# Kernel optimization log

Measured on AMD Instinct MI355X. Metric: run time of the kernel, lower is better.

## Reference

```python
import jax, jax.numpy as jnp
import numpy as np

N_HEAD = 16
ROPE_BASE = 10000.0

def rotate_half(x):
    half = x.shape[-1] // 2
    return jnp.concatenate((-x[..., half:], x[..., :half]), axis=-1)

def rope_freqs(T, head_dim, dtype):
    inv_freq = 1.0 / (ROPE_BASE ** (jnp.arange(0, head_dim, 2, dtype=jnp.float32) / head_dim))
    t = jnp.arange(T, dtype=jnp.float32)
    freqs = t[:, None] * inv_freq[None, :]          # [T, head_dim//2]
    emb = jnp.concatenate((freqs, freqs), axis=-1)  # [T, head_dim]
    return emb.astype(dtype)

def setup_inputs() -> dict:
    key = jax.random.key(0)
    ks = jax.random.split(key, 9)
    B, T, C = 2, 2048, 1024
    s = 1.0 / np.sqrt(C)
    return {
        'x':  jax.random.normal(ks[0], (B, T, C), jnp.float32),
        'Wq': jax.random.normal(ks[1], (C, C), jnp.float32) * s,
        'bq': jnp.zeros((C,), jnp.float32),
        'Wk': jax.random.normal(ks[2], (C, C), jnp.float32) * s,
        'bk': jnp.zeros((C,), jnp.float32),
        'Wv': jax.random.normal(ks[3], (C, C), jnp.float32) * s,
        'bv': jnp.zeros((C,), jnp.float32),
        'Wp': jax.random.normal(ks[4], (C, C), jnp.float32) * s,
        'bp': jnp.zeros((C,), jnp.float32),
    }

def reference(x, Wq, bq, Wk, bk, Wv, bv, Wp, bp):
    B, T, C = x.shape
    H = N_HEAD
    D = C // H
    # torch Linear: y = x @ W.T + b
    def heads(y):
        return y.reshape(B, T, H, D).transpose(0, 2, 1, 3)  # [B,H,T,D]
    q = heads(x @ Wq.T + bq)
    k = heads(x @ Wk.T + bk)
    v = heads(x @ Wv.T + bv)
    # inline RoPE
    emb = rope_freqs(T, D, x.dtype)          # [T, D]
    cos, sin = jnp.cos(emb), jnp.sin(emb)
    q = q * cos + rotate_half(q) * sin
    k = k * cos + rotate_half(k) * sin
    # full T x T scores with causal masked softmax
    att = jnp.einsum('bhtd,bhsd->bhts', q, k) * (1.0 / jnp.sqrt(jnp.array(D, x.dtype)))
    causal = jnp.tril(jnp.ones((T, T), bool))
    att = jnp.where(causal[None, None], att, jnp.array(-jnp.inf, att.dtype))
    att = jax.nn.softmax(att, axis=-1)
    y = jnp.einsum('bhts,bhsd->bhtd', att, v)  # [B,H,T,D]
    y = y.transpose(0, 2, 1, 3).reshape(B, T, C)
    return y @ Wp.T + bp
```

## Files before the change

### kernel.cpp

```cpp
#include <hip/hip_runtime.h>
#include <hip/hip_bf16.h>
#include <stdint.h>

typedef unsigned short u16;
typedef __attribute__((ext_vector_type(8))) short bf16x8;
typedef __attribute__((ext_vector_type(4))) float f32x4;
typedef __attribute__((ext_vector_type(2))) unsigned int u32x2;

typedef const __attribute__((address_space(1))) unsigned int* gu32p;
typedef __attribute__((address_space(3))) unsigned int* lu32p;

__device__ __forceinline__ void gl_lds16(const u16* g, u16* l) {
  __builtin_amdgcn_global_load_lds((gu32p)(const void*)g, (lu32p)(void*)l, 16, 0, 0);
}

template<int N> __device__ __forceinline__ void wait_vmcnt() {
  if constexpr (N == 0)      asm volatile("s_waitcnt vmcnt(0)" ::: "memory");
  else if constexpr (N == 3) asm volatile("s_waitcnt vmcnt(3)" ::: "memory");
  else if constexpr (N == 4) asm volatile("s_waitcnt vmcnt(4)" ::: "memory");
  else                       asm volatile("s_waitcnt vmcnt(6)" ::: "memory");
}

__device__ __forceinline__ u16 f2bf(float f) {
  union { float f; unsigned u; } v; v.f = f;
  unsigned r = v.u + 0x7fffu + ((v.u >> 16) & 1u);
  return (u16)(r >> 16);
}
__device__ __forceinline__ void st2bf(u16* p0, u16* p1, float a, float b) {
  union { __hip_bfloat162 h; u16 u[2]; } cv;
  cv.h = __float22bfloat162_rn(make_float2(a, b));
  *p0 = cv.u[0]; *p1 = cv.u[1];
}
__device__ __forceinline__ unsigned pk2bf(float a, float b) {
  union { __hip_bfloat162 h; unsigned u; } cv;
  cv.h = __float22bfloat162_rn(make_float2(a, b));
  return cv.u;
}

__global__ void convert_kernel(const float4* __restrict__ x, const float4* __restrict__ wq,
                               const float4* __restrict__ wk, const float4* __restrict__ wv,
                               const float4* __restrict__ wp,
                               u16* __restrict__ xb, u16* __restrict__ wqb, u16* __restrict__ wkb,
                               u16* __restrict__ wvb, u16* __restrict__ wpb,
                               float2* __restrict__ tab) {
  int i = blockIdx.x * 256 + threadIdx.x;
  const int NX = 1048576, NW = 262144, NCONV = NX + 4 * NW;
  if (i >= NCONV) {
    int j = i - NCONV;
    int d = j & 31, t = j >> 5;
    float ang = (float)t * expf(-0.28782313662425572f * (float)d);
    tab[j] = make_float2(cosf(ang), sinf(ang));
    return;
  }
  const float4* src; u16* dst; int off;
  if (i < NX)            { src = x;  dst = xb;  off = i; }
  else if (i < NX + NW)  { src = wq; dst = wqb; off = i - NX; }
  else if (i < NX + 2*NW){ src = wk; dst = wkb; off = i - NX - NW; }
  else if (i < NX + 3*NW){ src = wv; dst = wvb; off = i - NX - 2*NW; }
  else                   { src = wp; dst = wpb; off = i - NX - 3*NW; }
  float4 v = src[off];
  ushort4 ov = make_ushort4(f2bf(v.x), f2bf(v.y), f2bf(v.z), f2bf(v.w));
  *(ushort4*)&dst[off * 4] = ov;
}

template<int FUSE_ROPE, int OUT_BF16, int TRANS_V, int BM, int BN, int BK, int NZ>
__global__ __launch_bounds__(256) void gemm_bt_kernel(
    const u16* __restrict__ A,
    const u16* __restrict__ B0, const u16* __restrict__ B1, const u16* __restrict__ B2,
    const float* __restrict__ bias0, const float* __restrict__ bias1, const float* __restrict__ bias2,
    void* out0, void* out1, void* out2, const float2* __restrict__ tab)
{
  const int MT = BM / 32, NT = BN / 32;
  const int LOADS = (BK == 32) ? (BM/64 + BN/64) : (BM/32 + BN/32);
  const int NSTEP = 1024 / BK;
  __shared__ __align__(16) u16 As[3][BM * BK];
  __shared__ __align__(16) u16 Bs[3][BN * BK];

  const int NXg = 1024 / BN, NYg = 4096 / BM;
  const int nwg = NXg * NYg * NZ;
  const int wgid = blockIdx.x + NXg * (blockIdx.y + NYg * blockIdx.z);
  const int swz = (wgid & 7) * (nwg >> 3) + (wgid >> 3);
  const int bx = swz % NXg, by = (swz / NXg) % NYg, z = swz / (NXg * NYg);

  const u16* Bw = (z == 0) ? B0 : (z == 1) ? B1 : B2;
  const float* bias = (z == 0) ? bias0 : (z == 1) ? bias1 : bias2;
  void* outv = (z == 0) ? out0 : (z == 1) ? out1 : out2;
  const int tid = threadIdx.x, lane = tid & 63, w = tid >> 6;
  const int wr = w >> 1, wc = w & 1;
  const int quad = lane >> 4, l15 = lane & 15;
  const int m0 = by * BM, n0 = bx * BN;
  const int sr = lane >> 2;
  const int sg = ((lane & 3) ^ ((lane >> 3) & 3)) * 8;
  const int sr64 = lane >> 3;
  const int sg64 = ((lane & 7) ^ (lane >> 3)) * 8;
  const int rg4 = (l15 >> 1) & 3;

  auto stg = [&](int kt, int bf) {
    const int k0 = kt * BK;
    if constexpr (BK == 32) {
      #pragma unroll
      for (int p = 0; p < BM/64; p++)
        gl_lds16(A  + (m0 + p*64 + w*16 + sr) * 1024 + k0 + sg, &As[bf][p*2048 + w*512]);
      #pragma unroll
      for (int p = 0; p < BN/64; p++)
        gl_lds16(Bw + (n0 + p*64 + w*16 + sr) * 1024 + k0 + sg, &Bs[bf][p*2048 + w*512]);
    } else {
      #pragma unroll
      for (int p = 0; p < BM/32; p++)
        gl_lds16(A  + (m0 + p*32 + w*8 + sr64) * 1024 + k0 + sg64, &As[bf][p*2048 + w*512]);
      #pragma unroll
      for (int p = 0; p < BN/32; p++)
        gl_lds16(Bw + (n0 + p*32 + w*8 + sr64) * 1024 + k0 + sg64, &Bs[bf][p*2048 + w*512]);
    }
  };

  f32x4 acc[MT][NT] = {};
  stg(0, 0);
  stg(1, 1);
  int cur = 0;
  for (int kt = 0; kt < NSTEP; kt++) {
    __builtin_amdgcn_sched_barrier(0);
    if (kt < NSTEP-1) wait_vmcnt<LOADS>();
    else              wait_vmcnt<0>();
    __builtin_amdgcn_sched_barrier(0);
    __builtin_amdgcn_s_barrier();
    __builtin_amdgcn_sched_barrier(0);
    if (kt < NSTEP-2) stg(kt + 2, cur == 0 ? 2 : cur - 1);
    const int bf = cur;
    if constexpr (BK == 32) {
      bf16x8 af[MT], bfr[NT];
      #pragma unroll
      for (int mt = 0; mt < MT; mt++)
        af[mt] = *(const bf16x8*)&As[bf][(wr*(BM/2) + mt*16 + l15) * 32 + (quad ^ rg4) * 8];
      #pragma unroll
      for (int nt = 0; nt < NT; nt++)
        bfr[nt] = *(const bf16x8*)&Bs[bf][(wc*(BN/2) + nt*16 + l15) * 32 + (quad ^ rg4) * 8];
      #pragma unroll
      for (int mt = 0; mt < MT; mt++)
        #pragma unroll
        for (int nt = 0; nt < NT; nt++)
          acc[mt][nt] = __builtin_amdgcn_mfma_f32_16x16x32_bf16(af[mt], bfr[nt], acc[mt][nt], 0, 0, 0);
    } else {
      #pragma unroll
      for (int kk = 0; kk < 2; kk++) {
        bf16x8 af[MT], bfr[NT];
        #pragma unroll
        for (int mt = 0; mt < MT; mt++)
          af[mt] = *(const bf16x8*)&As[bf][(wr*(BM/2) + mt*16 + l15) * 64 + ((kk*4 + quad) ^ (l15 & 7)) * 8];
        #pragma unroll
        for (int nt = 0; nt < NT; nt++)
          bfr[nt] = *(const bf16x8*)&Bs[bf][(wc*(BN/2) + nt*16 + l15) * 64 + ((kk*4 + quad) ^ (l15 & 7)) * 8];
        #pragma unroll
        for (int mt = 0; mt < MT; mt++)
          #pragma unroll
          for (int nt = 0; nt < NT; nt++)
            acc[mt][nt] = __builtin_amdgcn_mfma_f32_16x16x32_bf16(af[mt], bfr[nt], acc[mt][nt], 0, 0, 0);
      }
    }
    cur = (cur == 2) ? 0 : cur + 1;
  }

  if (TRANS_V && z == 2) {
    const int bb = m0 >> 11, tg0 = (m0 & 2047) + wr*(BM/2) + quad*4;
    #pragma unroll
    for (int nt = 0; nt < NT; nt++) {
      const int c = n0 + wc*(BN/2) + nt*16 + l15;
      const float bv = bias[c];
      u16* vrow = (u16*)outv + (size_t)(bb*1024 + c) * 2048 + tg0;
      #pragma unroll
      for (int mt = 0; mt < MT; mt++) {
        ushort4 pk;
        pk.x = f2bf(acc[mt][nt][0] + bv); pk.y = f2bf(acc[mt][nt][1] + bv);
        pk.z = f2bf(acc[mt][nt][2] + bv); pk.w = f2bf(acc[mt][nt][3] + bv);
        *(ushort4*)&vrow[mt*16] = pk;
      }
    }
    return;
  }

  #pragma unroll
  for (int mt = 0; mt < MT; mt++) {
    #pragma unroll
    for (int r = 0; r < 4; r++) {
      const int row = m0 + wr*(BM/2) + mt*16 + quad*4 + r;
      float v[NT];
      #pragma unroll
      for (int nt = 0; nt < NT; nt++)
        v[nt] = acc[mt][nt][r] + bias[n0 + wc*(BN/2) + nt*16 + l15];
      if (FUSE_ROPE && z < 2) {
        const int t = row & 2047;
        #pragma unroll
        for (int nt = 0; nt < 2; nt++) {
          const int d = nt*16 + l15;
          float2 cs = tab[t*32 + d];
          float x0 = v[nt], x1 = v[nt+2];
          v[nt]   = x0 * cs.x - x1 * cs.y;
          v[nt+2] = x1 * cs.x + x0 * cs.y;
        }
        if (z == 0) {
          const float SC = 0.18033688011112042f;
          #pragma unroll
          for (int nt = 0; nt < NT; nt++) v[nt] *= SC;
        }
      }
      #pragma unroll
      for (int nt = 0; nt < NT; nt++) {
        const int col = n0 + wc*(BN/2) + nt*16 + l15;
        if (OUT_BF16) ((u16*)outv)[row * 1024 + col] = f2bf(v[nt]);
        else          ((float*)outv)[row * 1024 + col] = v[nt];
      }
    }
  }
}

__global__ __launch_bounds__(256) void attn_kernel(
    const u16* __restrict__ qg, const u16* __restrict__ kg,
    const u16* __restrict__ vtg, u16* __restrict__ yg)
{
  __shared__ __align__(16) u16 K_lds[2][64 * 64];
  __shared__ __align__(16) u16 V_lds[2][64 * 64];
  const int x = blockIdx.x;
  const int hh = blockIdx.y, b = blockIdx.z;
  const int t = b ? x : (31 - x);
  const int tid = threadIdx.x, lane = tid & 63, w = tid >> 6;
  const int quad = lane >> 4, l15 = lane & 15;
  const int bh = b * (2048 * 1024) + hh * 64;
  const int vtb = (b * 16 + hh) * 131072;

  bf16x8 qf[2];
  const int qrow = t*64 + w*16 + l15;
  qf[0] = *(const bf16x8*)&qg[bh + qrow*1024 + quad*8];
  qf[1] = *(const bf16x8*)&qg[bh + qrow*1024 + 32 + quad*8];

  f32x4 o[4] = {};
  f32x4 l5 = {};

  bf16x8 ones;
  #pragma unroll
  for (int i2 = 0; i2 < 8; i2++) ones[i2] = (short)0x3F80;

  auto do_stage = [&](int j, int bf) {
    #pragma unroll
    for (int p = 0; p < 2; p++) {
      const int seg = w*2 + p;
      const int r = seg*8 + (lane >> 3);
      const int g = (lane & 7) ^ (r & 7);
      gl_lds16(kg + bh + (j*64 + r) * 1024 + g*8, &K_lds[bf][seg*512]);
    }
    #pragma unroll
    for (int p = 0; p < 2; p++) {
      const int seg = w*2 + p;
      const int r = seg*8 + (lane >> 3);
      const int g = (lane & 7) ^ (r & 7);
      gl_lds16(vtg + vtb + r * 2048 + j*64 + g*8, &V_lds[bf][seg*512]);
    }
  };

  do_stage(0, 0);
  for (int j = 0; j <= t; j++) {
    __syncthreads();
    if (j < t) do_stage(j + 1, (j + 1) & 1);
    const int bf = j & 1;
    const bool diag = (j == t);

    #pragma unroll
    for (int ss = 0; ss < 2; ss++) {
      f32x4 s[2];
      #pragma unroll
      for (int h = 0; h < 2; h++) {
        const int nt = ss*2 + h;
        const int krow = (nt*16 + l15) * 64;
        const int g0 = ((quad)     ^ (l15 & 7)) * 8;
        const int g1 = ((4 + quad) ^ (l15 & 7)) * 8;
        bf16x8 kf0 = *(const bf16x8*)&K_lds[bf][krow + g0];
        bf16x8 kf1 = *(const bf16x8*)&K_lds[bf][krow + g1];
        __builtin_amdgcn_s_setprio(1);
        f32x4 z = {};
        z = __builtin_amdgcn_mfma_f32_16x16x32_bf16(kf0, qf[0], z, 0, 0, 0);
        z = __builtin_amdgcn_mfma_f32_16x16x32_bf16(kf1, qf[1], z, 0, 0, 0);
        s[h] = z;
        __builtin_amdgcn_s_setprio(0);
      }
      if (diag) {
        const int qr = w*16 + l15;
        #pragma unroll
        for (int h = 0; h < 2; h++)
          #pragma unroll
          for (int r = 0; r < 4; r++)
            if ((ss*2 + h)*16 + quad*4 + r > qr) s[h][r] = -1e30f;
      }
      float a0 = __builtin_amdgcn_exp2f(s[0][0]), a1 = __builtin_amdgcn_exp2f(s[0][1]);
      float a2 = __builtin_amdgcn_exp2f(s[0][2]), a3 = __builtin_amdgcn_exp2f(s[0][3]);
      float b0 = __builtin_amdgcn_exp2f(s[1][0]), b1 = __builtin_amdgcn_exp2f(s[1][1]);
      float b2 = __builtin_amdgcn_exp2f(s[1][2]), b3 = __builtin_amdgcn_exp2f(s[1][3]);
      unsigned A01 = pk2bf(a0, a1), A23 = pk2bf(a2, a3);
      unsigned B01 = pk2bf(b0, b1), B23 = pk2bf(b2, b3);
      u32x2 t0 = __builtin_amdgcn_permlane32_swap(A01, B01, false, false);
      u32x2 w02 = __builtin_amdgcn_permlane16_swap(t0[0], t0[1], false, false);
      u32x2 t1 = __builtin_amdgcn_permlane32_swap(A23, B23, false, false);
      u32x2 w13 = __builtin_amdgcn_permlane16_swap(t1[0], t1[1], false, false);
      union { unsigned u[4]; bf16x8 v; } pk;
      pk.u[0] = w02[0]; pk.u[1] = w13[0]; pk.u[2] = w02[1]; pk.u[3] = w13[1];
      bf16x8 pa = pk.v;
      __builtin_amdgcn_s_setprio(1);
      l5 = __builtin_amdgcn_mfma_f32_16x16x32_bf16(pa, ones, l5, 0, 0, 0);
      #pragma unroll
      for (int dt = 0; dt < 4; dt++) {
        const int vg = ((ss*4 + quad) ^ (l15 & 7)) * 8;
        bf16x8 vf = *(const bf16x8*)&V_lds[bf][(dt*16 + l15)*64 + vg];
        o[dt] = __builtin_amdgcn_mfma_f32_16x16x32_bf16(pa, vf, o[dt], 0, 0, 0);
      }
      __builtin_amdgcn_s_setprio(0);
    }
  }

  #pragma unroll
  for (int r = 0; r < 4; r++) {
    float inv = 1.0f / l5[r];
    u16* yr = &yg[bh + (t*64 + w*16 + quad*4 + r) * 1024 + l15];
    st2bf(yr,      yr + 16, o[0][r] * inv, o[1][r] * inv);
    st2bf(yr + 32, yr + 48, o[2][r] * inv, o[3][r] * inv);
  }
}

extern "C" void kernel_launch(void* const* d_in, const int* in_sizes, int n_in,
                              void* d_out, int out_size, void* d_ws, size_t ws_size,
                              hipStream_t stream) {
  const float* x  = (const float*)d_in[0];
  const float* Wq = (const float*)d_in[1];
  const float* bq = (const float*)d_in[2];
  const float* Wk = (const float*)d_in[3];
  const float* bk = (const float*)d_in[4];
  const float* Wv = (const float*)d_in[5];
  const float* bv = (const float*)d_in[6];
  const float* Wp = (const float*)d_in[7];
  const float* bp = (const float*)d_in[8];

  char* ws = (char*)d_ws;
  u16* xb  = (u16*)(ws);
  u16* wqb = (u16*)(ws + (8u  << 20));
  u16* wkb = (u16*)(ws + (10u << 20));
  u16* wvb = (u16*)(ws + (12u << 20));
  u16* wpb = (u16*)(ws + (14u << 20));
  u16* qb  = (u16*)(ws + (16u << 20));
  u16* kb  = (u16*)(ws + (24u << 20));
  u16* vtb = (u16*)(ws + (32u << 20));
  float2* tab = (float2*)(ws + (40u << 20));
  u16* yb = xb;

  convert_kernel<<<8448, 256, 0, stream>>>((const float4*)x, (const float4*)Wq, (const float4*)Wk,
                                           (const float4*)Wv, (const float4*)Wp,
                                           xb, wqb, wkb, wvb, wpb, tab);
  gemm_bt_kernel<1, 1, 1, 128, 128, 32, 3><<<dim3(8, 32, 3), 256, 0, stream>>>(
      xb, wqb, wkb, wvb, bq, bk, bv, (void*)qb, (void*)kb, (void*)vtb, tab);
  attn_kernel<<<dim3(32, 16, 2), 256, 0, stream>>>(qb, kb, vtb, yb);
  gemm_bt_kernel<0, 0, 0, 128, 64, 64, 1><<<dim3(16, 32, 1), 256, 0, stream>>>(
      yb, wpb, wpb, wpb, bp, bp, bp, (void*)d_out, (void*)d_out, (void*)d_out, tab);
}
```

Baseline: 183.1 us.

## Fuse Q/K/V projections into one GEMM sharing A tiles across three weights

Replaces the z-batched QKV GEMM (768 workgroups of 128x128 tiles, one weight per block) with a dedicated kernel in which each 128-row x 64-column block loads one A tile and the matching 64-row slices of Wq, Wk and Wv. Each A tile is then reused across three weight matrices, cutting A re-reads, and the grid drops to 512 blocks. The RoPE, scale and transposed-V epilogues move into this kernel. In exchange each block holds 24 accumulator tiles, which raises register pressure and may lower occupancy, and the fewer, larger blocks change how work spreads across CUs.

```diff
diff --git a/kernel.cpp b/kernel.cpp
--- a/kernel.cpp
+++ b/kernel.cpp
@@ -18,6 +18,7 @@
   if constexpr (N == 0)      asm volatile("s_waitcnt vmcnt(0)" ::: "memory");
   else if constexpr (N == 3) asm volatile("s_waitcnt vmcnt(3)" ::: "memory");
   else if constexpr (N == 4) asm volatile("s_waitcnt vmcnt(4)" ::: "memory");
+  else if constexpr (N == 5) asm volatile("s_waitcnt vmcnt(5)" ::: "memory");
   else                       asm volatile("s_waitcnt vmcnt(6)" ::: "memory");
 }
 
@@ -63,12 +64,115 @@
   *(ushort4*)&dst[off * 4] = ov;
 }
 
-template<int FUSE_ROPE, int OUT_BF16, int TRANS_V, int BM, int BN, int BK, int NZ>
+__global__ __launch_bounds__(256) void gemm_qkv_fused(
+    const u16* __restrict__ A,
+    const u16* __restrict__ W0, const u16* __restrict__ W1, const u16* __restrict__ W2,
+    const float* __restrict__ bq, const float* __restrict__ bk, const float* __restrict__ bv,
+    u16* __restrict__ qo, u16* __restrict__ ko, u16* __restrict__ vto,
+    const float2* __restrict__ tab)
+{
+  __shared__ __align__(16) u16 As[3][128 * 32];
+  __shared__ __align__(16) u16 Bs[3][3 * 64 * 32];
+
+  const int wgid = blockIdx.x + 16 * blockIdx.y;
+  const int swz = (wgid & 7) * 64 + (wgid >> 3);
+  const int bx = swz & 15, by = swz >> 4;
+
+  const int tid = threadIdx.x, lane = tid & 63, w = tid >> 6;
+  const int wr = w >> 1, wc = w & 1;
+  const int quad = lane >> 4, l15 = lane & 15;
+  const int m0 = by * 128, n0 = bx * 64;
+  const int sr = lane >> 2;
+  const int sg = ((lane & 3) ^ ((lane >> 3) & 3)) * 8;
+  const int rg4 = (l15 >> 1) & 3;
+
+  auto stg = [&](int kt, int bf) {
+    const int k0 = kt * 32;
+    #pragma unroll
+    for (int p = 0; p < 2; p++)
+      gl_lds16(A + (m0 + p*64 + w*16 + sr) * 1024 + k0 + sg, &As[bf][p*2048 + w*512]);
+    gl_lds16(W0 + (n0 + w*16 + sr) * 1024 + k0 + sg, &Bs[bf][0*2048 + w*512]);
+    gl_lds16(W1 + (n0 + w*16 + sr) * 1024 + k0 + sg, &Bs[bf][1*2048 + w*512]);
+    gl_lds16(W2 + (n0 + w*16 + sr) * 1024 + k0 + sg, &Bs[bf][2*2048 + w*512]);
+  };
+
+  f32x4 acc[4][6] = {};
+  stg(0, 0);
+  stg(1, 1);
+  int cur = 0;
+  for (int kt = 0; kt < 32; kt++) {
+    __builtin_amdgcn_sched_barrier(0);
+    if (kt < 31) wait_vmcnt<5>();
+    else         wait_vmcnt<0>();
+    __builtin_amdgcn_sched_barrier(0);
+    __builtin_amdgcn_s_barrier();
+    __builtin_amdgcn_sched_barrier(0);
+    if (kt < 30) stg(kt + 2, cur == 0 ? 2 : cur - 1);
+    const int bf = cur;
+    bf16x8 af[4], bfr[6];
+    #pragma unroll
+    for (int mt = 0; mt < 4; mt++)
+      af[mt] = *(const bf16x8*)&As[bf][(wr*64 + mt*16 + l15) * 32 + (quad ^ rg4) * 8];
+    #pragma unroll
+    for (int zz = 0; zz < 3; zz++)
+      #pragma unroll
+      for (int nt = 0; nt < 2; nt++)
+        bfr[zz*2+nt] = *(const bf16x8*)&Bs[bf][zz*2048 + (nt*32 + wc*16 + l15) * 32 + (quad ^ rg4) * 8];
+    #pragma unroll
+    for (int mt = 0; mt < 4; mt++)
+      #pragma unroll
+      for (int f = 0; f < 6; f++)
+        acc[mt][f] = __builtin_amdgcn_mfma_f32_16x16x32_bf16(af[mt], bfr[f], acc[mt][f], 0, 0, 0);
+    cur = (cur == 2) ? 0 : cur + 1;
+  }
+
+  const int d = wc*16 + l15;
+  #pragma unroll
+  for (int zz = 0; zz < 2; zz++) {
+    u16* outp = zz ? ko : qo;
+    const float* bias = zz ? bk : bq;
+    const float b0 = bias[n0 + d], b1 = bias[n0 + 32 + d];
+    #pragma unroll
+    for (int mt = 0; mt < 4; mt++)
+      #pragma unroll
+      for (int r = 0; r < 4; r++) {
+        const int row = m0 + wr*64 + mt*16 + quad*4 + r;
+        const int t = row & 2047;
+        float2 cs = tab[t*32 + d];
+        float x0 = acc[mt][zz*2+0][r] + b0;
+        float x1 = acc[mt][zz*2+1][r] + b1;
+        float v0 = x0 * cs.x - x1 * cs.y;
+        float v1 = x1 * cs.x + x0 * cs.y;
+        if (zz == 0) {
+          const float SC = 0.18033688011112042f;
+          v0 *= SC; v1 *= SC;
+        }
+        outp[row * 1024 + n0 + d]      = f2bf(v0);
+        outp[row * 1024 + n0 + 32 + d] = f2bf(v1);
+      }
+  }
+  {
+    const int bb = m0 >> 11, tg0 = (m0 & 2047) + wr*64 + quad*4;
+    #pragma unroll
+    for (int nt = 0; nt < 2; nt++) {
+      const int c = n0 + nt*32 + wc*16 + l15;
+      const float bvv = bv[c];
+      u16* vrow = vto + (size_t)(bb*1024 + c) * 2048 + tg0;
+      #pragma unroll
+      for (int mt = 0; mt < 4; mt++) {
+        ushort4 pk;
+        pk.x = f2bf(acc[mt][4+nt][0] + bvv); pk.y = f2bf(acc[mt][4+nt][1] + bvv);
+        pk.z = f2bf(acc[mt][4+nt][2] + bvv); pk.w = f2bf(acc[mt][4+nt][3] + bvv);
+        *(ushort4*)&vrow[mt*16] = pk;
+      }
+    }
+  }
+}
+
+template<int OUT_BF16, int BM, int BN, int BK, int NZ>
 __global__ __launch_bounds__(256) void gemm_bt_kernel(
-    const u16* __restrict__ A,
-    const u16* __restrict__ B0, const u16* __restrict__ B1, const u16* __restrict__ B2,
-    const float* __restrict__ bias0, const float* __restrict__ bias1, const float* __restrict__ bias2,
-    void* out0, void* out1, void* out2, const float2* __restrict__ tab)
+    const u16* __restrict__ A, const u16* __restrict__ B0,
+    const float* __restrict__ bias0, void* out0)
 {
   const int MT = BM / 32, NT = BN / 32;
   const int LOADS = (BK == 32) ? (BM/64 + BN/64) : (BM/32 + BN/32);
@@ -80,11 +184,11 @@
   const int nwg = NXg * NYg * NZ;
   const int wgid = blockIdx.x + NXg * (blockIdx.y + NYg * blockIdx.z);
   const int swz = (wgid & 7) * (nwg >> 3) + (wgid >> 3);
-  const int bx = swz % NXg, by = (swz / NXg) % NYg, z = swz / (NXg * NYg);
-
-  const u16* Bw = (z == 0) ? B0 : (z == 1) ? B1 : B2;
-  const float* bias = (z == 0) ? bias0 : (z == 1) ? bias1 : bias2;
-  void* outv = (z == 0) ? out0 : (z == 1) ? out1 : out2;
+  const int bx = swz % NXg, by = (swz / NXg) % NYg;
+
+  const u16* Bw = B0;
+  const float* bias = bias0;
+  void* outv = out0;
   const int tid = threadIdx.x, lane = tid & 63, w = tid >> 6;
   const int wr = w >> 1, wc = w & 1;
   const int quad = lane >> 4, l15 = lane & 15;
@@ -160,24 +264,6 @@
     cur = (cur == 2) ? 0 : cur + 1;
   }
 
-  if (TRANS_V && z == 2) {
-    const int bb = m0 >> 11, tg0 = (m0 & 2047) + wr*(BM/2) + quad*4;
-    #pragma unroll
-    for (int nt = 0; nt < NT; nt++) {
-      const int c = n0 + wc*(BN/2) + nt*16 + l15;
-      const float bv = bias[c];
-      u16* vrow = (u16*)outv + (size_t)(bb*1024 + c) * 2048 + tg0;
-      #pragma unroll
-      for (int mt = 0; mt < MT; mt++) {
-        ushort4 pk;
-        pk.x = f2bf(acc[mt][nt][0] + bv); pk.y = f2bf(acc[mt][nt][1] + bv);
-        pk.z = f2bf(acc[mt][nt][2] + bv); pk.w = f2bf(acc[mt][nt][3] + bv);
-        *(ushort4*)&vrow[mt*16] = pk;
-      }
-    }
-    return;
-  }
-
   #pragma unroll
   for (int mt = 0; mt < MT; mt++) {
     #pragma unroll
@@ -187,22 +273,6 @@
       #pragma unroll
       for (int nt = 0; nt < NT; nt++)
         v[nt] = acc[mt][nt][r] + bias[n0 + wc*(BN/2) + nt*16 + l15];
-      if (FUSE_ROPE && z < 2) {
-        const int t = row & 2047;
-        #pragma unroll
-        for (int nt = 0; nt < 2; nt++) {
-          const int d = nt*16 + l15;
-          float2 cs = tab[t*32 + d];
-          float x0 = v[nt], x1 = v[nt+2];
-          v[nt]   = x0 * cs.x - x1 * cs.y;
-          v[nt+2] = x1 * cs.x + x0 * cs.y;
-        }
-        if (z == 0) {
-          const float SC = 0.18033688011112042f;
-          #pragma unroll
-          for (int nt = 0; nt < NT; nt++) v[nt] *= SC;
-        }
-      }
       #pragma unroll
       for (int nt = 0; nt < NT; nt++) {
         const int col = n0 + wc*(BN/2) + nt*16 + l15;
@@ -351,9 +421,9 @@
   convert_kernel<<<8448, 256, 0, stream>>>((const float4*)x, (const float4*)Wq, (const float4*)Wk,
                                            (const float4*)Wv, (const float4*)Wp,
                                            xb, wqb, wkb, wvb, wpb, tab);
-  gemm_bt_kernel<1, 1, 1, 128, 128, 32, 3><<<dim3(8, 32, 3), 256, 0, stream>>>(
-      xb, wqb, wkb, wvb, bq, bk, bv, (void*)qb, (void*)kb, (void*)vtb, tab);
+  gemm_qkv_fused<<<dim3(16, 32), 256, 0, stream>>>(
+      xb, wqb, wkb, wvb, bq, bk, bv, qb, kb, vtb, tab);
   attn_kernel<<<dim3(32, 16, 2), 256, 0, stream>>>(qb, kb, vtb, yb);
-  gemm_bt_kernel<0, 0, 0, 128, 64, 64, 1><<<dim3(16, 32, 1), 256, 0, stream>>>(
-      yb, wpb, wpb, wpb, bp, bp, bp, (void*)d_out, (void*)d_out, (void*)d_out, tab);
-}
+  gemm_bt_kernel<0, 128, 64, 64, 1><<<dim3(16, 32, 1), 256, 0, stream>>>(
+      yb, wpb, bp, (void*)d_out);
+}
```

After: 182.9 us, median of 3. Within noise of the previous version (-0.1%).
